# Performance work log

Measured on AMD Instinct MI355X. Metric: run time of the kernel, lower is better.

## Reference

```python
import jax, jax.numpy as jnp
import numpy as np

N = 32768      # nodes
E = 524288     # edges (avg degree 16)
F = 64         # node_feat_dim
D = 64         # gnn_dim (= per-head out channels, concat=False)
ED = 32        # edge_feat_dim
L = 6          # num_layers
H = 2          # heads
C = D          # per-head channels
LN_EPS = 1e-5


def layer_norm(h, g, b):
    mu = jnp.mean(h, axis=-1, keepdims=True)
    var = jnp.mean((h - mu) ** 2, axis=-1, keepdims=True)
    return g * (h - mu) * jax.lax.rsqrt(var + LN_EPS) + b


def setup_inputs() -> dict:
    key = jax.random.key(0)
    ks = jax.random.split(key, 16)
    x = jax.random.normal(ks[0], (N, F), jnp.float32)
    edge_index = jax.random.randint(ks[1], (2, E), 0, N, jnp.int32)
    edge_attr = jax.random.normal(ks[2], (E, ED), jnp.float32)
    manual_gamma = 1.0 + 0.1 * jax.random.normal(ks[3], (L, D), jnp.float32)
    manual_beta = 0.1 * jax.random.normal(ks[4], (L, D), jnp.float32)
    # node_embed Linear(F, D)
    embed_W = jax.random.normal(ks[5], (F, D), jnp.float32) / np.float32(np.sqrt(F))
    embed_b = jnp.zeros((D,), jnp.float32)
    # per-layer LayerNorm affine params
    ln_gamma = jnp.ones((L, D), jnp.float32)
    ln_beta = jnp.zeros((L, D), jnp.float32)
    # per-layer GATConv params (shared lin for src/dst, PyG non-bipartite)
    lin_W = jax.random.normal(ks[6], (L, D, H * C), jnp.float32) / np.float32(np.sqrt(D))
    lin_edge_W = jax.random.normal(ks[7], (L, ED, H * C), jnp.float32) / np.float32(np.sqrt(ED))
    att_src = jax.random.normal(ks[8], (L, H, C), jnp.float32) / np.float32(np.sqrt(C))
    att_dst = jax.random.normal(ks[9], (L, H, C), jnp.float32) / np.float32(np.sqrt(C))
    att_edge = jax.random.normal(ks[10], (L, H, C), jnp.float32) / np.float32(np.sqrt(C))
    gat_bias = jnp.zeros((L, C), jnp.float32)
    # edge output head: Linear(2D+ED, D) -> ReLU -> Linear(D, 1)
    head_W1 = jax.random.normal(ks[11], (2 * D + ED, D), jnp.float32) / np.float32(np.sqrt(2 * D + ED))
    head_b1 = jnp.zeros((D,), jnp.float32)
    head_W2 = jax.random.normal(ks[12], (D, 1), jnp.float32) / np.float32(np.sqrt(D))
    head_b2 = jnp.zeros((1,), jnp.float32)
    return dict(x=x, edge_index=edge_index, edge_attr=edge_attr,
                manual_gamma=manual_gamma, manual_beta=manual_beta,
                embed_W=embed_W, embed_b=embed_b, ln_gamma=ln_gamma, ln_beta=ln_beta,
                lin_W=lin_W, lin_edge_W=lin_edge_W, att_src=att_src, att_dst=att_dst,
                att_edge=att_edge, gat_bias=gat_bias, head_W1=head_W1, head_b1=head_b1,
                head_W2=head_W2, head_b2=head_b2)


def reference(x, edge_index, edge_attr, manual_gamma, manual_beta,
              embed_W, embed_b, ln_gamma, ln_beta, lin_W, lin_edge_W,
              att_src, att_dst, att_edge, gat_bias, head_W1, head_b1,
              head_W2, head_b2):
    src, dst = edge_index[0], edge_index[1]
    # PyG GATConv default add_self_loops=True, fill_value='mean' for edge_attr
    loop = jnp.arange(N, dtype=edge_index.dtype)
    src_f = jnp.concatenate([src, loop])   # [E+N]
    dst_f = jnp.concatenate([dst, loop])
    deg = jax.ops.segment_sum(jnp.ones((E,), x.dtype), dst, num_segments=N)
    loop_attr = jax.ops.segment_sum(edge_attr, dst, num_segments=N) / jnp.maximum(deg, 1.0)[:, None]
    edge_attr_f = jnp.concatenate([edge_attr, loop_attr], axis=0)  # [E+N, ED]

    h = x @ embed_W + embed_b  # [N, D]
    for l in range(L):
        hn = layer_norm(h, ln_gamma[l], ln_beta[l])
        hm = manual_gamma[l][None, :] * hn + manual_beta[l][None, :]
        xh = (hm @ lin_W[l]).reshape(N, H, C)                      # [N,H,C]
        a_s = jnp.sum(xh * att_src[l][None], axis=-1)              # [N,H]
        a_d = jnp.sum(xh * att_dst[l][None], axis=-1)              # [N,H]
        eh = (edge_attr_f @ lin_edge_W[l]).reshape(-1, H, C)       # [E+N,H,C]
        a_e = jnp.sum(eh * att_edge[l][None], axis=-1)             # [E+N,H]
        alpha = jax.nn.leaky_relu(a_s[src_f] + a_d[dst_f] + a_e, 0.2)
        amax = jax.ops.segment_max(alpha, dst_f, num_segments=N)   # every node has a self-loop
        ex = jnp.exp(alpha - amax[dst_f])
        den = jax.ops.segment_sum(ex, dst_f, num_segments=N)
        w = ex / (den[dst_f] + 1e-16)                              # segment softmax [E+N,H]
        msg = xh[src_f] * w[..., None]                             # [E+N,H,C]
        out = jax.ops.segment_sum(msg, dst_f, num_segments=N)      # [N,H,C]
        h = jax.nn.relu(jnp.mean(out, axis=1) + gat_bias[l])       # concat=False -> head mean

    ef = jnp.concatenate([h[src], h[dst], edge_attr], axis=-1)     # [E, 2D+ED]
    hid = jax.nn.relu(ef @ head_W1 + head_b1)
    return (hid @ head_W2 + head_b2)[:, 0]                         # [E]
```

## Files before the change

kernel.cpp:

```cpp
#include <hip/hip_runtime.h>
#include <hip/hip_bf16.h>
#include <math.h>

#define NN 32768
#define EE 524288
#define LL 6

typedef __attribute__((ext_vector_type(8))) short short8;
typedef __attribute__((ext_vector_type(4))) float floatx4;
typedef __attribute__((ext_vector_type(4))) float fx4;
typedef __attribute__((ext_vector_type(2))) float fx2;

union U16x8 { short8 v; unsigned short u[8]; };

__device__ __forceinline__ unsigned short f2bf(float x) {
    union { float f; unsigned int u; } v; v.f = x;
    unsigned int r = v.u + 0x7fffu + ((v.u >> 16) & 1u);
    return (unsigned short)(r >> 16);
}
__device__ __forceinline__ float bf2f(unsigned short h) {
    union { unsigned int u; float f; } v; v.u = (unsigned int)h << 16;
    return v.f;
}


__global__ void deg_kernel(const int* __restrict__ dst, int* __restrict__ deg) {
    int i = (blockIdx.x * 256 + threadIdx.x) * 4;
    int4 d = *(const int4*)(dst + i);
    atomicAdd(&deg[d.x], 1);
    atomicAdd(&deg[d.y], 1);
    atomicAdd(&deg[d.z], 1);
    atomicAdd(&deg[d.w], 1);
}

__global__ __launch_bounds__(1024) void scan_kernel(const int* __restrict__ deg,
                                                    int* __restrict__ row_ptr,
                                                    int* __restrict__ cnt) {
    __shared__ int bs[1024];
    int t = threadIdx.x;
    int base = t * 32;
    int loc[32];
    int s = 0;
#pragma unroll
    for (int i = 0; i < 32; ++i) { int v = deg[base + i]; loc[i] = s; s += v; }
    bs[t] = s;
    __syncthreads();
    for (int off = 1; off < 1024; off <<= 1) {
        int v = (t >= off) ? bs[t - off] : 0;
        __syncthreads();
        bs[t] += v;
        __syncthreads();
    }
    int pre = (t == 0) ? 0 : bs[t - 1];
#pragma unroll
    for (int i = 0; i < 32; ++i) { row_ptr[base + i] = pre + loc[i]; cnt[base + i] = 0; }
    if (t == 1023) row_ptr[NN] = bs[1023];
}

__global__ void fill_kernel(const int* __restrict__ src, const int* __restrict__ dst,
                            const int* __restrict__ row_ptr, int* __restrict__ cnt,
                            int2* __restrict__ sedge) {
    int e = blockIdx.x * 256 + threadIdx.x;
    if (e >= EE) return;
    int d = dst[e];
    int pos = row_ptr[d] + atomicAdd(&cnt[d], 1);
    sedge[pos] = make_int2(e, src[e]);
}

__global__ __launch_bounds__(256) void smallprep_kernel(
    const float* __restrict__ lin_W, const float* __restrict__ head_W1,
    const float* __restrict__ lin_edge_W, const float* __restrict__ att_edge,
    const float* __restrict__ att_src, const float* __restrict__ att_dst,
    unsigned short* __restrict__ gBhi, unsigned short* __restrict__ gBlo,
    unsigned short* __restrict__ aeBhi, unsigned short* __restrict__ aeBlo,
    float* __restrict__ vs, float* __restrict__ vvd,
    unsigned short* __restrict__ w1chi, unsigned short* __restrict__ w1clo,
    int* __restrict__ deg) {
    __shared__ float svb[384];
    int bb = blockIdx.x;
    int tid = threadIdx.x;
    if (bb < 7) {
        unsigned short* dh = gBhi + (size_t)bb * 128 * 64;
        unsigned short* dl = gBlo + (size_t)bb * 128 * 64;
        if (bb < 6) {
            int n2 = tid & 63, kh = tid >> 6;
            U16x8 hh[4], ll[4];
            for (int kk = 0; kk < 32; ++kk) {
                int j = kh * 32 + kk;
                int h = j >> 6, k = j & 63;
                float wv = 0.5f * lin_W[((size_t)bb * 64 + k) * 128 + h * 64 + n2];
                unsigned short h16 = f2bf(wv);
                hh[kk >> 3].u[kk & 7] = h16;
                ll[kk >> 3].u[kk & 7] = f2bf(wv - bf2f(h16));
            }
#pragma unroll
            for (int c = 0; c < 4; ++c) {
                int cg = kh * 4 + c;
                int off = n2 * 128 + ((cg ^ (n2 & 15)) << 3);
                *(short8*)(dh + off) = hh[c].v;
                *(short8*)(dl + off) = ll[c].v;
            }
        } else {
            int n = tid & 127, kh = tid >> 7;
            U16x8 hh[4], ll[4];
            for (int kk = 0; kk < 32; ++kk) {
                int k = kh * 32 + kk;
                float wv = (n < 64) ? head_W1[k * 64 + n] : head_W1[(64 + k) * 64 + (n - 64)];
                unsigned short h16 = f2bf(wv);
                hh[kk >> 3].u[kk & 7] = h16;
                ll[kk >> 3].u[kk & 7] = f2bf(wv - bf2f(h16));
            }
#pragma unroll
            for (int c = 0; c < 4; ++c) {
                int cg = kh * 4 + c;
                int off = n * 64 + ((cg ^ (n & 7)) << 3);
                *(short8*)(dh + off) = hh[c].v;
                *(short8*)(dl + off) = ll[c].v;
            }
        }
    } else if (bb == 7) {
        for (int t = tid; t < 384; t += 256) {
            int l = t / 64; int r = t & 63; int ed = r >> 1; int hh = r & 1;
            const float* w = lin_edge_W + l * 32 * 128 + ed * 128 + hh * 64;
            const float* a = att_edge + l * 128 + hh * 64;
            float s = 0.f;
#pragma unroll 8
            for (int c = 0; c < 64; ++c) s += w[c] * a[c];
            svb[t] = s;
        }
        int n = tid & 63, kc = tid >> 6;
#pragma unroll
        for (int j = 0; j < 8; ++j) {
            int k = kc * 8 + j;
            float wv = head_W1[(128 + k) * 64 + n];
            unsigned short h16 = f2bf(wv);
            w1chi[n * 32 + k] = h16;
            w1clo[n * 32 + k] = f2bf(wv - bf2f(h16));
        }
        __syncthreads();
        if (tid < 64) {
            int n2 = tid & 15, q = tid >> 4;
            U16x8 hi, lo;
#pragma unroll
            for (int i = 0; i < 8; ++i) {
                int k = q * 8 + i;
                float val = (n2 < 12) ? svb[(n2 >> 1) * 64 + k * 2 + (n2 & 1)] : 0.f;
                unsigned short h16 = f2bf(val);
                hi.u[i] = h16;
                lo.u[i] = f2bf(val - bf2f(h16));
            }
            *(short8*)(aeBhi + tid * 8) = hi.v;
            *(short8*)(aeBlo + tid * 8) = lo.v;
        }
    } else if (bb < 14) {
        int l = bb - 8;
        int sel = tid >> 7, idx = tid & 127;
        int h = idx >> 6, k = idx & 63;
        const float* att = (sel ? att_dst : att_src) + l * 128 + h * 64;
        const float* wr = lin_W + ((size_t)l * 64 + k) * 128 + h * 64;
        float s = 0.f;
#pragma unroll 8
        for (int c = 0; c < 64; ++c) s += wr[c] * att[c];
        (sel ? vvd : vs)[l * 128 + idx] = s;
    } else {
        int i = (bb - 14) * 1024 + tid * 4;
        *(int4*)(deg + i) = make_int4(0, 0, 0, 0);
    }
}

__global__ __launch_bounds__(256) void ae_csr_kernel(
    const float* __restrict__ edge_attr, const int2* __restrict__ sedge,
    const unsigned short* __restrict__ aeBhi, const unsigned short* __restrict__ aeBlo,
    float* __restrict__ aeF, int* __restrict__ srcc) {
    __shared__ float tr[4][64 * 13];
    int tid = threadIdx.x;
    int w = tid >> 6, lane = tid & 63;
    int p0 = blockIdx.x * 256 + w * 64;
    short8 bhi = *(const short8*)(aeBhi + lane * 8);
    short8 blo = *(const short8*)(aeBlo + lane * 8);
    int r = lane & 15, q = lane >> 4;
    float* trw = tr[w];
#pragma unroll
    for (int t = 0; t < 4; ++t) {
        int eg = sedge[p0 + t * 16 + r].x;
        const fx4* p = (const fx4*)(edge_attr + (size_t)eg * 32 + q * 8);
        fx4 f0 = p[0], f1 = p[1];
        float av[8] = {f0.x, f0.y, f0.z, f0.w, f1.x, f1.y, f1.z, f1.w};
        U16x8 hi, lo;
#pragma unroll
        for (int jj = 0; jj < 8; ++jj) {
            unsigned short h16 = f2bf(av[jj]);
            hi.u[jj] = h16;
            lo.u[jj] = f2bf(av[jj] - bf2f(h16));
        }
        floatx4 acc = {};
        acc = __builtin_amdgcn_mfma_f32_16x16x32_bf16(lo.v, bhi, acc, 0, 0, 0);
        acc = __builtin_amdgcn_mfma_f32_16x16x32_bf16(hi.v, blo, acc, 0, 0, 0);
        acc = __builtin_amdgcn_mfma_f32_16x16x32_bf16(hi.v, bhi, acc, 0, 0, 0);
        if (r < 12) {
#pragma unroll
            for (int rr = 0; rr < 4; ++rr)
                trw[(t * 16 + q * 4 + rr) * 13 + r] = acc[rr];
        }
    }
    int2 sl = sedge[p0 + lane];
    srcc[p0 + lane] = sl.y;
#pragma unroll
    for (int l = 0; l < LL; ++l) {
        fx2 rec;
        rec.x = trw[lane * 13 + l * 2];
        rec.y = trw[lane * 13 + l * 2 + 1];
        __builtin_nontemporal_store(rec, (fx2*)(aeF + ((size_t)l * EE + p0 + lane) * 2));
    }
}

__global__ __launch_bounds__(256) void embed_ln_kernel(
    const float* __restrict__ x, const float* __restrict__ W, const float* __restrict__ b,
    const float* __restrict__ ln_g, const float* __restrict__ ln_b,
    const float* __restrict__ mg, const float* __restrict__ mb,
    const float* __restrict__ vs0, const float* __restrict__ vd0,
    unsigned short* __restrict__ hm_bf, float* __restrict__ a_s, float* __restrict__ a_d) {
    __shared__ float xr[4][64];
    int w = threadIdx.x >> 6, j = threadIdx.x & 63;
    int n = blockIdx.x * 4 + w;
    xr[w][j] = x[(size_t)n * 64 + j];
    __syncthreads();
    float acc = b[j];
#pragma unroll 8
    for (int k = 0; k < 64; ++k) acc += xr[w][k] * W[k * 64 + j];
    float s = acc, sq = acc * acc;
    for (int off = 1; off < 64; off <<= 1) { s += __shfl_xor(s, off); sq += __shfl_xor(sq, off); }
    float mu = s * (1.f / 64.f);
    float var = sq * (1.f / 64.f) - mu * mu;
    float rs = rsqrtf(var + 1e-5f);
    float hm = mg[j] * (ln_g[j] * (acc - mu) * rs + ln_b[j]) + mb[j];
    hm_bf[(size_t)n * 64 + j] = f2bf(hm);
    float s0 = hm * vs0[j], s1 = hm * vs0[64 + j];
    float d0 = hm * vd0[j], d1 = hm * vd0[64 + j];
    for (int off = 1; off < 64; off <<= 1) {
        s0 += __shfl_xor(s0, off); s1 += __shfl_xor(s1, off);
        d0 += __shfl_xor(d0, off); d1 += __shfl_xor(d1, off);
    }
    if (j == 0) {
        a_s[n * 2] = s0; a_s[n * 2 + 1] = s1;
        a_d[n * 2] = d0; a_d[n * 2 + 1] = d1;
    }
}

__device__ __forceinline__ void fma8h(uint4 pv, float w, float* a) {
    unsigned int u[4] = {pv.x, pv.y, pv.z, pv.w};
#pragma unroll
    for (int q = 0; q < 4; ++q) {
        union { unsigned int x; float f; } lo, hi;
        lo.x = u[q] << 16; hi.x = u[q] & 0xffff0000u;
        a[2 * q]     += w * lo.f;
        a[2 * q + 1] += w * hi.f;
    }
}

__device__ __forceinline__ void agg_node(
    int n, int ch, int hh, int j, const uint4* hmv, const float2* as2,
    const float* ad_in, const float* aeLl, const int* srcc,
    const int* row_ptr, float* sg, U16x8& hb) {
    float2 adn = ((const float2*)ad_in)[n];
    float2 asn = as2[n];
    uint4 pvself = hmv[(size_t)n * 8 + ch];
    int beg = row_ptr[n], end = row_ptr[n + 1];
    int degn = end - beg;
    float acc[8] = {};
    float den = 0.f, aex = 0.f, aey = 0.f;
    for (int base = 0; base < degn; base += 32) {
        int cnt = degn - base; cnt = cnt > 32 ? 32 : cnt;
        int nchunk = (cnt + 15) >> 4;
        for (int it = 0; it < nchunk; ++it) {
            int s0 = it * 16;
            int rem = cnt - s0;
            float w0v = 0.f, w1v = 0.f;
            int sval = 0;
            if (j < rem) {
                int idx = beg + base + s0 + j;
                int sv = srcc[idx];
                fx2 ae = *(const fx2*)(aeLl + (size_t)idx * 2);
                float2 as = as2[sv];
                aex += ae.x; aey += ae.y;
                float al0 = as.x + adn.x + ae.x; al0 = al0 > 0.f ? al0 : 0.2f * al0;
                float al1 = as.y + adn.y + ae.y; al1 = al1 > 0.f ? al1 : 0.2f * al1;
                w0v = __expf(al0);
                w1v = __expf(al1);
                sval = sv;
            }
            float4 st;
            st.x = __int_as_float(sval); st.y = w0v; st.z = w1v; st.w = 0.f;
            *(float4*)(sg + (s0 + j) * 4) = st;
        }
        int c8 = (cnt + 7) & ~7;
        for (int s = 0; s < c8; s += 8) {
            float4 m[8];
#pragma unroll
            for (int u = 0; u < 8; ++u) m[u] = *(const float4*)(sg + (s + u) * 4);
            uint4 p[8];
#pragma unroll
            for (int u = 0; u < 8; ++u) p[u] = hmv[(size_t)__float_as_int(m[u].x) * 8 + ch];
#pragma unroll
            for (int u = 0; u < 8; ++u) {
                float b = hh ? m[u].z : m[u].y;
                den += b;
                fma8h(p[u], b, acc);
            }
        }
    }
#pragma unroll
    for (int m = 1; m < 16; m <<= 1) {
        aex += __shfl_xor(aex, m);
        aey += __shfl_xor(aey, m);
    }
    float invd = 1.f / fmaxf((float)degn, 1.f);
    float al0 = asn.x + adn.x + aex * invd; al0 = al0 > 0.f ? al0 : 0.2f * al0;
    float al1 = asn.y + adn.y + aey * invd; al1 = al1 > 0.f ? al1 : 0.2f * al1;
    float ws = hh ? __expf(al1) : __expf(al0);
    den += ws;
    fma8h(pvself, ws, acc);
    float inv = 1.f / (den + 1e-16f);
#pragma unroll
    for (int q = 0; q < 8; ++q) hb.u[q] = f2bf(acc[q] * inv);
}

__global__ __launch_bounds__(512) void fused_post(
    const unsigned short* __restrict__ hm_in, const float* __restrict__ as_in,
    const float* __restrict__ ad_in, const float* __restrict__ aeLl,
    const int* __restrict__ srcc, const int* __restrict__ row_ptr,
    const unsigned short* __restrict__ gBhi, const unsigned short* __restrict__ gBlo,
    const float* __restrict__ bias, const float* __restrict__ ln_g,
    const float* __restrict__ ln_b, const float* __restrict__ mg,
    const float* __restrict__ mb, const float* __restrict__ vsn,
    const float* __restrict__ vdn, unsigned short* __restrict__ hm_out,
    float* __restrict__ as_out, float* __restrict__ ad_out) {
    __shared__ char smem[49152];
    unsigned short* Ahi = (unsigned short*)smem;
    float* stgAll = (float*)(smem + 16384);
    unsigned short* Bhi = (unsigned short*)(smem + 16384);
    unsigned short* Blo = (unsigned short*)(smem + 32768);
    int tid = threadIdx.x;
    int w = tid >> 6, lane = tid & 63;
    int g = lane >> 4, j = lane & 15;
    int ch = j & 7, hh = j >> 3;
    const float2* as2 = (const float2*)as_in;
    const uint4* hmv = (const uint4*)hm_in;
    float* sg = stgAll + (w * 4 + g) * 128;
    int nb = blockIdx.x * 64;

    for (int rr = 0; rr < 2; ++rr) {
        int m = w * 8 + rr * 4 + g;
        U16x8 hb;
        agg_node(nb + m, ch, hh, j, hmv, as2, ad_in, aeLl, srcc, row_ptr, sg, hb);
        int cg = hh * 8 + ch;
        *(short8*)(Ahi + m * 128 + ((cg ^ (m & 15)) << 3)) = hb.v;
    }
    __syncthreads();
    {
        const uint4* sh = (const uint4*)gBhi;
        const uint4* sl = (const uint4*)gBlo;
        for (int i = tid; i < 1024; i += 512) {
            ((uint4*)Bhi)[i] = sh[i];
            ((uint4*)Blo)[i] = sl[i];
        }
    }
    __syncthreads();

    if (w < 4) {
        int col = lane & 15, quad = lane >> 4;
        int m = w * 16 + col;
        floatx4 acc[4] = {};
#pragma unroll
        for (int s = 0; s < 4; ++s) {
            int ca = (quad + 4 * s) ^ col;
            short8 ahi = *(const short8*)(Ahi + m * 128 + ca * 8);
#pragma unroll
            for (int t = 0; t < 4; ++t) {
                int off = (t * 16 + col) * 128 + ca * 8;
                short8 bhi = *(const short8*)(Bhi + off);
                short8 blo = *(const short8*)(Blo + off);
                acc[t] = __builtin_amdgcn_mfma_f32_16x16x32_bf16(ahi, blo, acc[t], 0, 0, 0);
                acc[t] = __builtin_amdgcn_mfma_f32_16x16x32_bf16(ahi, bhi, acc[t], 0, 0, 0);
            }
        }
        int nodebase = nb + w * 16;
        float bv[4];
#pragma unroll
        for (int t = 0; t < 4; ++t) bv[t] = bias[t * 16 + col];
        float vsv[4], vsv1[4], vdv[4], vdv1[4], lg[4], lb[4], mgv[4], mbv[4];
#pragma unroll
        for (int t = 0; t < 4; ++t) {
            int c = t * 16 + col;
            vsv[t] = vsn[c]; vsv1[t] = vsn[64 + c];
            vdv[t] = vdn[c]; vdv1[t] = vdn[64 + c];
            lg[t] = ln_g[c]; lb[t] = ln_b[c];
            mgv[t] = mg[c]; mbv[t] = mb[c];
        }
#pragma unroll
        for (int r = 0; r < 4; ++r) {
            int node = nodebase + quad * 4 + r;
            float hv[4];
            float s = 0.f, sq = 0.f;
#pragma unroll
            for (int t = 0; t < 4; ++t) {
                float v = acc[t][r] + bv[t];
                v = v > 0.f ? v : 0.f;
                hv[t] = v;
                s += v; sq += v * v;
            }
            for (int off = 1; off < 16; off <<= 1) { s += __shfl_xor(s, off); sq += __shfl_xor(sq, off); }
            float mu = s * (1.f / 64.f);
            float var = sq * (1.f / 64.f) - mu * mu;
            float rs = rsqrtf(var + 1e-5f);
            float s0 = 0.f, s1 = 0.f, d0 = 0.f, d1 = 0.f;
#pragma unroll
            for (int t = 0; t < 4; ++t) {
                float hmval = mgv[t] * (lg[t] * (hv[t] - mu) * rs + lb[t]) + mbv[t];
                hm_out[(size_t)node * 64 + t * 16 + col] = f2bf(hmval);
                s0 += hmval * vsv[t]; s1 += hmval * vsv1[t];
                d0 += hmval * vdv[t]; d1 += hmval * vdv1[t];
            }
            for (int off = 1; off < 16; off <<= 1) {
                s0 += __shfl_xor(s0, off); s1 += __shfl_xor(s1, off);
                d0 += __shfl_xor(d0, off); d1 += __shfl_xor(d1, off);
            }
            if (col == 0) {
                as_out[node * 2] = s0; as_out[node * 2 + 1] = s1;
                ad_out[node * 2] = d0; ad_out[node * 2 + 1] = d1;
            }
        }
    }
}

__global__ __launch_bounds__(512) void fused_uv(
    const unsigned short* __restrict__ hm_in, const float* __restrict__ as_in,
    const float* __restrict__ ad_in, const float* __restrict__ aeLl,
    const int* __restrict__ srcc, const int* __restrict__ row_ptr,
    const unsigned short* __restrict__ gB5hi, const unsigned short* __restrict__ gB5lo,
    const float* __restrict__ bias,
    const unsigned short* __restrict__ gB6hi, const unsigned short* __restrict__ gB6lo,
    unsigned short* __restrict__ uv) {
    __shared__ char smem[49152];
    unsigned short* Ahi  = (unsigned short*)smem;
    float* stgAll        = (float*)(smem + 16384);
    unsigned short* B5hi = (unsigned short*)(smem + 16384);
    unsigned short* B5lo = (unsigned short*)(smem + 32768);
    unsigned short* A2hi = (unsigned short*)smem;
    unsigned short* A2lo = (unsigned short*)(smem + 8192);
    unsigned short* B6hi = (unsigned short*)(smem + 16384);
    unsigned short* B6lo = (unsigned short*)(smem + 32768);
    int tid = threadIdx.x;
    int w = tid >> 6, lane = tid & 63;
    int g = lane >> 4, j = lane & 15;
    int ch = j & 7, hh = j >> 3;
    const float2* as2 = (const float2*)as_in;
    const uint4* hmv = (const uint4*)hm_in;
    float* sg = stgAll + (w * 4 + g) * 128;
    int nb = blockIdx.x * 64;

    for (int rr = 0; rr < 2; ++rr) {
        int m = w * 8 + rr * 4 + g;
        U16x8 hb;
        agg_node(nb + m, ch, hh, j, hmv, as2, ad_in, aeLl, srcc, row_ptr, sg, hb);
        int cg = hh * 8 + ch;
        *(short8*)(Ahi + m * 128 + ((cg ^ (m & 15)) << 3)) = hb.v;
    }
    __syncthreads();
    {
        const uint4* sh = (const uint4*)gB5hi;
        const uint4* sl = (const uint4*)gB5lo;
        for (int i = tid; i < 1024; i += 512) {
            ((uint4*)B5hi)[i] = sh[i];
            ((uint4*)B5lo)[i] = sl[i];
        }
    }
    __syncthreads();

    int col = lane & 15, quad = lane >> 4;
    int m = w * 16 + col;
    floatx4 acc[4] = {};
    if (w < 4) {
#pragma unroll
        for (int s = 0; s < 4; ++s) {
            int ca = (quad + 4 * s) ^ col;
            short8 ahi = *(const short8*)(Ahi + m * 128 + ca * 8);
#pragma unroll
            for (int t = 0; t < 4; ++t) {
                int off = (t * 16 + col) * 128 + ca * 8;
                short8 bhi = *(const short8*)(B5hi + off);
                short8 blo = *(const short8*)(B5lo + off);
                acc[t] = __builtin_amdgcn_mfma_f32_16x16x32_bf16(ahi, blo, acc[t], 0, 0, 0);
                acc[t] = __builtin_amdgcn_mfma_f32_16x16x32_bf16(ahi, bhi, acc[t], 0, 0, 0);
            }
        }
    }
    __syncthreads();
    if (w < 4) {
        float bv[4];
#pragma unroll
        for (int t = 0; t < 4; ++t) bv[t] = bias[t * 16 + col];
#pragma unroll
        for (int t = 0; t < 4; ++t) {
            int c = t * 16 + col;
            int cg = c >> 3, cr = c & 7;
#pragma unroll
            for (int r = 0; r < 4; ++r) {
                float v = acc[t][r] + bv[t];
                v = v > 0.f ? v : 0.f;
                int i = w * 16 + quad * 4 + r;
                int off = i * 64 + ((cg ^ (i & 7)) << 3) + cr;
                unsigned short hhv = f2bf(v);
                A2hi[off] = hhv;
                A2lo[off] = f2bf(v - bf2f(hhv));
            }
        }
    }
    for (int i = tid; i < 1024; i += 512) {
        ((uint4*)B6hi)[i] = ((const uint4*)gB6hi)[i];
        ((uint4*)B6lo)[i] = ((const uint4*)gB6lo)[i];
    }
    __syncthreads();

    if (w < 4) {
        floatx4 acc2[8] = {};
#pragma unroll
        for (int s = 0; s < 2; ++s) {
            int ca = (quad + 4 * s) ^ (col & 7);
            short8 a2h = *(const short8*)(A2hi + m * 64 + ca * 8);
            short8 a2l = *(const short8*)(A2lo + m * 64 + ca * 8);
#pragma unroll
            for (int t = 0; t < 8; ++t) {
                int off = (t * 16 + col) * 64 + ca * 8;
                short8 bh = *(const short8*)(B6hi + off);
                short8 bl = *(const short8*)(B6lo + off);
                acc2[t] = __builtin_amdgcn_mfma_f32_16x16x32_bf16(a2l, bh, acc2[t], 0, 0, 0);
                acc2[t] = __builtin_amdgcn_mfma_f32_16x16x32_bf16(a2h, bl, acc2[t], 0, 0, 0);
                acc2[t] = __builtin_amdgcn_mfma_f32_16x16x32_bf16(a2h, bh, acc2[t], 0, 0, 0);
            }
        }
        int nodebase = nb + w * 16;
#pragma unroll
        for (int t = 0; t < 8; ++t)
#pragma unroll
            for (int r = 0; r < 4; ++r)
                uv[(size_t)(nodebase + quad * 4 + r) * 128 + t * 16 + col] = f2bf(acc2[t][r]);
    }
}

__global__ __launch_bounds__(256) void head2_kernel(
    const unsigned short* __restrict__ uv, const int* __restrict__ src,
    const int* __restrict__ dst, const float* __restrict__ edge_attr,
    const unsigned short* __restrict__ w1chi, const unsigned short* __restrict__ w1clo,
    const float* __restrict__ b1, const float* __restrict__ W2,
    const float* __restrict__ b2, float* __restrict__ out) {
    __shared__ float g[64][68];
    __shared__ unsigned short Abf[64 * 40];
    __shared__ unsigned short Bh[64 * 40], Bl[64 * 40];
    __shared__ int sA[64], dA[64];
    int tid = threadIdx.x;
    int base = blockIdx.x * 64;
    if (tid < 64) sA[tid] = src[base + tid];
    else if (tid < 128) dA[tid - 64] = dst[base + tid - 64];
    {
        int n = tid >> 2, c = tid & 3;
        *(short8*)(Bh + n * 40 + c * 8) = *(const short8*)(w1chi + n * 32 + c * 8);
        *(short8*)(Bl + n * 40 + c * 8) = *(const short8*)(w1clo + n * 32 + c * 8);
    }
    {
        int e = tid >> 2, q = tid & 3;
        const fx4* p = (const fx4*)(edge_attr + (size_t)(base + e) * 32 + q * 8);
        fx4 f0 = __builtin_nontemporal_load(p);
        fx4 f1 = __builtin_nontemporal_load(p + 1);
        float av[8] = {f0.x, f0.y, f0.z, f0.w, f1.x, f1.y, f1.z, f1.w};
        U16x8 cv;
#pragma unroll
        for (int jj = 0; jj < 8; ++jj) cv.u[jj] = f2bf(av[jj]);
        *(short8*)(Abf + e * 40 + q * 8) = cv.v;
    }
    __syncthreads();
    {
        int e = tid >> 2, q = tid & 3;
        const uint4* su = (const uint4*)(uv + (size_t)sA[e] * 128);
        const uint4* dv = (const uint4*)(uv + (size_t)dA[e] * 128);
        uint4 U0 = su[2 * q], U1 = su[2 * q + 1];
        uint4 V0 = dv[8 + 2 * q], V1 = dv[9 + 2 * q];
        const float4* b1p = (const float4*)(b1 + q * 16);
        float bb[16];
#pragma unroll
        for (int jj = 0; jj < 4; ++jj) {
            float4 b4 = b1p[jj];
            bb[4 * jj] = b4.x; bb[4 * jj + 1] = b4.y; bb[4 * jj + 2] = b4.z; bb[4 * jj + 3] = b4.w;
        }
        unsigned int uw[8] = {U0.x, U0.y, U0.z, U0.w, U1.x, U1.y, U1.z, U1.w};
        unsigned int vw[8] = {V0.x, V0.y, V0.z, V0.w, V1.x, V1.y, V1.z, V1.w};
        float* gr = &g[e][q * 16];
#pragma unroll
        for (int jj = 0; jj < 8; ++jj) {
            gr[2 * jj] = bf2f((unsigned short)(uw[jj] & 0xffff)) +
                         bf2f((unsigned short)(vw[jj] & 0xffff)) + bb[2 * jj];
            gr[2 * jj + 1] = bf2f((unsigned short)(uw[jj] >> 16)) +
                             bf2f((unsigned short)(vw[jj] >> 16)) + bb[2 * jj + 1];
        }
    }
    __syncthreads();

    int lane = tid & 63, w = tid >> 6, col = lane & 15, quad = lane >> 4;
    short8 a = *(const short8*)(Abf + (w * 16 + col) * 40 + quad * 8);
    floatx4 acc[4] = {};
#pragma unroll
    for (int t = 0; t < 4; ++t) {
        int off = (t * 16 + col) * 40 + quad * 8;
        short8 bh = *(const short8*)(Bh + off);
        short8 bl = *(const short8*)(Bl + off);
        acc[t] = __builtin_amdgcn_mfma_f32_16x16x32_bf16(a, bl, acc[t], 0, 0, 0);
        acc[t] = __builtin_amdgcn_mfma_f32_16x16x32_bf16(a, bh, acc[t], 0, 0, 0);
    }
    float sv[4] = {0.f, 0.f, 0.f, 0.f};
#pragma unroll
    for (int t = 0; t < 4; ++t) {
        float w2v = W2[t * 16 + col];
#pragma unroll
        for (int r = 0; r < 4; ++r) {
            float hid = acc[t][r] + g[w * 16 + quad * 4 + r][t * 16 + col];
            hid = hid > 0.f ? hid : 0.f;
            sv[r] += hid * w2v;
        }
    }
    float b2v = b2[0];
#pragma unroll
    for (int r = 0; r < 4; ++r) {
        float v = sv[r];
        v += __shfl_xor(v, 1);
        v += __shfl_xor(v, 2);
        v += __shfl_xor(v, 4);
        v += __shfl_xor(v, 8);
        if (col == 0) out[base + w * 16 + quad * 4 + r] = v + b2v;
    }
}


extern "C" void kernel_launch(void* const* d_in, const int* in_sizes, int n_in,
                              void* d_out, int out_size, void* d_ws, size_t ws_size,
                              hipStream_t stream) {
    const float* x            = (const float*)d_in[0];
    const int*   edge_index   = (const int*)d_in[1];
    const float* edge_attr    = (const float*)d_in[2];
    const float* manual_gamma = (const float*)d_in[3];
    const float* manual_beta  = (const float*)d_in[4];
    const float* embed_W      = (const float*)d_in[5];
    const float* embed_b      = (const float*)d_in[6];
    const float* ln_gamma     = (const float*)d_in[7];
    const float* ln_beta      = (const float*)d_in[8];
    const float* lin_W        = (const float*)d_in[9];
    const float* lin_edge_W   = (const float*)d_in[10];
    const float* att_src      = (const float*)d_in[11];
    const float* att_dst      = (const float*)d_in[12];
    const float* att_edge     = (const float*)d_in[13];
    const float* gat_bias     = (const float*)d_in[14];
    const float* head_W1      = (const float*)d_in[15];
    const float* head_b1      = (const float*)d_in[16];
    const float* head_W2      = (const float*)d_in[17];
    const float* head_b2      = (const float*)d_in[18];
    float* out = (float*)d_out;

    const int* src = edge_index;
    const int* dst = edge_index + EE;

    char* ws = (char*)d_ws;
    size_t off = 0;
    auto alloc = [&](size_t bytes) {
        void* p = ws + off;
        off += (bytes + 255) & ~(size_t)255;
        return p;
    };
    int*   deg        = (int*)alloc(NN * 4);
    int*   row_ptr    = (int*)alloc((NN + 1) * 4);
    int*   cnt        = (int*)alloc(NN * 4);
    int2*  sedge      = (int2*)alloc((size_t)EE * 8);
    int*   srcc       = (int*)alloc((size_t)EE * 4);
    float* aeF        = (float*)alloc((size_t)LL * EE * 8);
    float* vs         = (float*)alloc(LL * 128 * 4);
    float* vvd        = (float*)alloc(LL * 128 * 4);
    float* asA        = (float*)alloc((size_t)NN * 2 * 4);
    float* asB        = (float*)alloc((size_t)NN * 2 * 4);
    float* adA        = (float*)alloc((size_t)NN * 2 * 4);
    float* adB        = (float*)alloc((size_t)NN * 2 * 4);
    unsigned short* hmA   = (unsigned short*)alloc((size_t)NN * 64 * 2);
    unsigned short* hmB   = (unsigned short*)alloc((size_t)NN * 64 * 2);
    unsigned short* uvbuf = (unsigned short*)alloc((size_t)NN * 128 * 2);
    unsigned short* gBhi  = (unsigned short*)alloc((size_t)7 * 128 * 64 * 2);
    unsigned short* gBlo  = (unsigned short*)alloc((size_t)7 * 128 * 64 * 2);
    unsigned short* w1chi = (unsigned short*)alloc(64 * 32 * 2);
    unsigned short* w1clo = (unsigned short*)alloc(64 * 32 * 2);
    unsigned short* aeBhi = (unsigned short*)alloc(64 * 8 * 2);
    unsigned short* aeBlo = (unsigned short*)alloc(64 * 8 * 2);
    if (off > ws_size) return;

    smallprep_kernel<<<46, 256, 0, stream>>>(lin_W, head_W1, lin_edge_W, att_edge,
                                             att_src, att_dst, gBhi, gBlo, aeBhi, aeBlo,
                                             vs, vvd, w1chi, w1clo, deg);
    deg_kernel<<<EE / 1024, 256, 0, stream>>>(dst, deg);
    scan_kernel<<<1, 1024, 0, stream>>>(deg, row_ptr, cnt);
    fill_kernel<<<EE / 256, 256, 0, stream>>>(src, dst, row_ptr, cnt, sedge);
    ae_csr_kernel<<<EE / 256, 256, 0, stream>>>(edge_attr, sedge, aeBhi, aeBlo, aeF, srcc);
    embed_ln_kernel<<<NN / 4, 256, 0, stream>>>(x, embed_W, embed_b, ln_gamma, ln_beta,
                                                manual_gamma, manual_beta, vs, vvd,
                                                hmA, asA, adA);

    for (int l = 0; l < LL; ++l) {
        const unsigned short* hin = (l & 1) ? hmB : hmA;
        unsigned short* hout = (l & 1) ? hmA : hmB;
        const float* asi = (l & 1) ? asB : asA;
        float* aso = (l & 1) ? asA : asB;
        const float* adi = (l & 1) ? adB : adA;
        float* ado = (l & 1) ? adA : adB;
        const float* aeLl = aeF + (size_t)l * EE * 2;
        if (l < LL - 1) {
            fused_post<<<NN / 64, 512, 0, stream>>>(
                hin, asi, adi, aeLl, srcc, row_ptr,
                gBhi + (size_t)l * 128 * 64, gBlo + (size_t)l * 128 * 64,
                gat_bias + l * 64, ln_gamma + (l + 1) * 64, ln_beta + (l + 1) * 64,
                manual_gamma + (l + 1) * 64, manual_beta + (l + 1) * 64,
                vs + (l + 1) * 128, vvd + (l + 1) * 128, hout, aso, ado);
        } else {
            fused_uv<<<NN / 64, 512, 0, stream>>>(
                hin, asi, adi, aeLl, srcc, row_ptr,
                gBhi + (size_t)l * 128 * 64, gBlo + (size_t)l * 128 * 64,
                gat_bias + l * 64, gBhi + (size_t)6 * 128 * 64,
                gBlo + (size_t)6 * 128 * 64, uvbuf);
        }
    }

    head2_kernel<<<EE / 64, 256, 0, stream>>>(uvbuf, src, dst, edge_attr, w1chi, w1clo,
                                              head_b1, head_W2, head_b2, out);
}
```

Measured before the change: 423.7 us.

## Aggregate both heads per lane with 8 lanes per node instead of 16

The edge aggregation is remapped so each group of 8 lanes handles one node and each lane accumulates both attention heads for its 8-channel slice. Each gathered neighbour feature vector is reused for both heads, which halves the redundant gathers, and all 64 nodes of a block are covered in a single pass instead of two. The cost is twice the accumulator registers per lane and fewer lanes per node for the softmax-weight stage, so long-degree nodes now serialize more per group.

```diff
diff --git a/kernel.cpp b/kernel.cpp
--- a/kernel.cpp
+++ b/kernel.cpp
@@ -258,27 +258,26 @@
     }
 }
 
-__device__ __forceinline__ void agg_node(
-    int n, int ch, int hh, int j, const uint4* hmv, const float2* as2,
+__device__ __forceinline__ void agg_node2(
+    int n, int ch, const uint4* hmv, const float2* as2,
     const float* ad_in, const float* aeLl, const int* srcc,
-    const int* row_ptr, float* sg, U16x8& hb) {
+    const int* row_ptr, float* sg, U16x8& hb0, U16x8& hb1) {
     float2 adn = ((const float2*)ad_in)[n];
     float2 asn = as2[n];
     uint4 pvself = hmv[(size_t)n * 8 + ch];
     int beg = row_ptr[n], end = row_ptr[n + 1];
     int degn = end - beg;
-    float acc[8] = {};
-    float den = 0.f, aex = 0.f, aey = 0.f;
-    for (int base = 0; base < degn; base += 32) {
-        int cnt = degn - base; cnt = cnt > 32 ? 32 : cnt;
-        int nchunk = (cnt + 15) >> 4;
-        for (int it = 0; it < nchunk; ++it) {
-            int s0 = it * 16;
-            int rem = cnt - s0;
+    float acc0[8] = {}, acc1[8] = {};
+    float den0 = 0.f, den1 = 0.f, aex = 0.f, aey = 0.f;
+    for (int base = 0; base < degn; base += 16) {
+        int cnt = degn - base; cnt = cnt > 16 ? 16 : cnt;
+#pragma unroll
+        for (int pass = 0; pass < 2; ++pass) {
+            int s = pass * 8 + ch;
             float w0v = 0.f, w1v = 0.f;
             int sval = 0;
-            if (j < rem) {
-                int idx = beg + base + s0 + j;
+            if (s < cnt) {
+                int idx = beg + base + s;
                 int sv = srcc[idx];
                 fx2 ae = *(const fx2*)(aeLl + (size_t)idx * 2);
                 float2 as = as2[sv];
@@ -291,7 +290,7 @@
             }
             float4 st;
             st.x = __int_as_float(sval); st.y = w0v; st.z = w1v; st.w = 0.f;
-            *(float4*)(sg + (s0 + j) * 4) = st;
+            *(float4*)(sg + s * 4) = st;
         }
         int c8 = (cnt + 7) & ~7;
         for (int s = 0; s < c8; s += 8) {
@@ -303,26 +302,29 @@
             for (int u = 0; u < 8; ++u) p[u] = hmv[(size_t)__float_as_int(m[u].x) * 8 + ch];
 #pragma unroll
             for (int u = 0; u < 8; ++u) {
-                float b = hh ? m[u].z : m[u].y;
-                den += b;
-                fma8h(p[u], b, acc);
-            }
-        }
-    }
-#pragma unroll
-    for (int m = 1; m < 16; m <<= 1) {
-        aex += __shfl_xor(aex, m);
-        aey += __shfl_xor(aey, m);
+                den0 += m[u].y; fma8h(p[u], m[u].y, acc0);
+                den1 += m[u].z; fma8h(p[u], m[u].z, acc1);
+            }
+        }
+    }
+#pragma unroll
+    for (int m2 = 1; m2 < 8; m2 <<= 1) {
+        aex += __shfl_xor(aex, m2);
+        aey += __shfl_xor(aey, m2);
     }
     float invd = 1.f / fmaxf((float)degn, 1.f);
     float al0 = asn.x + adn.x + aex * invd; al0 = al0 > 0.f ? al0 : 0.2f * al0;
     float al1 = asn.y + adn.y + aey * invd; al1 = al1 > 0.f ? al1 : 0.2f * al1;
-    float ws = hh ? __expf(al1) : __expf(al0);
-    den += ws;
-    fma8h(pvself, ws, acc);
-    float inv = 1.f / (den + 1e-16f);
-#pragma unroll
-    for (int q = 0; q < 8; ++q) hb.u[q] = f2bf(acc[q] * inv);
+    float ws0 = __expf(al0), ws1 = __expf(al1);
+    den0 += ws0; den1 += ws1;
+    fma8h(pvself, ws0, acc0);
+    fma8h(pvself, ws1, acc1);
+    float inv0 = 1.f / (den0 + 1e-16f), inv1 = 1.f / (den1 + 1e-16f);
+#pragma unroll
+    for (int q = 0; q < 8; ++q) {
+        hb0.u[q] = f2bf(acc0[q] * inv0);
+        hb1.u[q] = f2bf(acc1[q] * inv1);
+    }
 }
 
 __global__ __launch_bounds__(512) void fused_post(
@@ -342,19 +344,18 @@
     unsigned short* Blo = (unsigned short*)(smem + 32768);
     int tid = threadIdx.x;
     int w = tid >> 6, lane = tid & 63;
-    int g = lane >> 4, j = lane & 15;
-    int ch = j & 7, hh = j >> 3;
+    int g = lane >> 3, ch = lane & 7;
     const float2* as2 = (const float2*)as_in;
     const uint4* hmv = (const uint4*)hm_in;
-    float* sg = stgAll + (w * 4 + g) * 128;
+    float* sg = stgAll + (w * 8 + g) * 64;
     int nb = blockIdx.x * 64;
 
-    for (int rr = 0; rr < 2; ++rr) {
-        int m = w * 8 + rr * 4 + g;
-        U16x8 hb;
-        agg_node(nb + m, ch, hh, j, hmv, as2, ad_in, aeLl, srcc, row_ptr, sg, hb);
-        int cg = hh * 8 + ch;
-        *(short8*)(Ahi + m * 128 + ((cg ^ (m & 15)) << 3)) = hb.v;
+    {
+        int m = w * 8 + g;
+        U16x8 hb0, hb1;
+        agg_node2(nb + m, ch, hmv, as2, ad_in, aeLl, srcc, row_ptr, sg, hb0, hb1);
+        *(short8*)(Ahi + m * 128 + ((ch ^ (m & 15)) << 3)) = hb0.v;
+        *(short8*)(Ahi + m * 128 + (((8 + ch) ^ (m & 15)) << 3)) = hb1.v;
     }
     __syncthreads();
     {
@@ -452,19 +453,18 @@
     unsigned short* B6lo = (unsigned short*)(smem + 32768);
     int tid = threadIdx.x;
     int w = tid >> 6, lane = tid & 63;
-    int g = lane >> 4, j = lane & 15;
-    int ch = j & 7, hh = j >> 3;
+    int g = lane >> 3, ch = lane & 7;
     const float2* as2 = (const float2*)as_in;
     const uint4* hmv = (const uint4*)hm_in;
-    float* sg = stgAll + (w * 4 + g) * 128;
+    float* sg = stgAll + (w * 8 + g) * 64;
     int nb = blockIdx.x * 64;
 
-    for (int rr = 0; rr < 2; ++rr) {
-        int m = w * 8 + rr * 4 + g;
-        U16x8 hb;
-        agg_node(nb + m, ch, hh, j, hmv, as2, ad_in, aeLl, srcc, row_ptr, sg, hb);
-        int cg = hh * 8 + ch;
-        *(short8*)(Ahi + m * 128 + ((cg ^ (m & 15)) << 3)) = hb.v;
+    {
+        int m = w * 8 + g;
+        U16x8 hb0, hb1;
+        agg_node2(nb + m, ch, hmv, as2, ad_in, aeLl, srcc, row_ptr, sg, hb0, hb1);
+        *(short8*)(Ahi + m * 128 + ((ch ^ (m & 15)) << 3)) = hb0.v;
+        *(short8*)(Ahi + m * 128 + (((8 + ch) ^ (m & 15)) << 3)) = hb1.v;
     }
     __syncthreads();
     {
```

Result: no change. 424.7 us (+0.2%).
